# Performance work log

Measured on AMD Instinct MI355X. Metric: run time of the kernel, lower is better.

The kernel has to match this reference:

```python
import jax, jax.numpy as jnp
import numpy as np
from jax import lax

DIM = 512
BATCH = 8
SEQ = 2048
LR = 0.1      # learning_rate (eta)
DECAY = 0.9   # decay_rate (lambda)


def setup_inputs() -> dict:
    key = jax.random.key(0)
    ks = jax.random.split(key, 5)
    scale = DIM ** -0.5
    return {
        "x": jax.random.normal(ks[0], (BATCH, SEQ, DIM), dtype=jnp.float32),
        "Wk": jax.random.normal(ks[1], (DIM, DIM), dtype=jnp.float32) * scale,
        "bk": jnp.zeros((DIM,), dtype=jnp.float32),
        "Wv": jax.random.normal(ks[2], (DIM, DIM), dtype=jnp.float32) * scale,
        "bv": jnp.zeros((DIM,), dtype=jnp.float32),
        "Wq": jax.random.normal(ks[3], (DIM, DIM), dtype=jnp.float32) * scale,
        "bq": jnp.zeros((DIM,), dtype=jnp.float32),
        "Wo": jax.random.normal(ks[4], (DIM, DIM), dtype=jnp.float32) * scale,
        "bo": jnp.zeros((DIM,), dtype=jnp.float32),
    }


def reference(x, Wk, bk, Wv, bv, Wq, bq, Wo, bo):
    B, S, D = x.shape
    # dense projections over all tokens at once
    k = x @ Wk + bk  # (B,S,D)
    v = x @ Wv + bv
    q = x @ Wq + bq

    state0 = jnp.zeros((B, D, D), dtype=x.dtype)

    def step(state, kvq):
        k_t, v_t, q_t = kvq                                  # each (B,D)
        mem = jnp.einsum('bd,bde->be', q_t, state)           # read BEFORE update
        new_state = DECAY * state + LR * jnp.einsum('bd,be->bde', k_t, v_t)
        return new_state, mem

    # scan over time: move seq axis to front
    kT = jnp.swapaxes(k, 0, 1)  # (S,B,D)
    vT = jnp.swapaxes(v, 0, 1)
    qT = jnp.swapaxes(q, 0, 1)
    final_state, mems = lax.scan(step, state0, (kT, vT, qT))  # mems (S,B,D)

    outputs = jnp.swapaxes(mems, 0, 1)                        # (B,S,D)
    out = outputs @ Wo + bo
    return out, final_state
```

## Files before the change

### kernel.cpp

```cpp
#include <hip/hip_runtime.h>
#include <math.h>


#define DIMD 512
#define SEQL 2048
#define LRC 0.1f
#define LAM64 1.1790184577738602e-3f
#define LAM128 1.3900845237714473e-6f
#define L2LAM -0.15200309344504997f

#define KVQ_ELEMS ((size_t)16384 * 512)
#define WSLAB ((size_t)512 * 512)

typedef __attribute__((ext_vector_type(8))) short bf16x8;
typedef __attribute__((ext_vector_type(4))) float f32x4;

__device__ __forceinline__ unsigned short f2bf(float f) {
  unsigned int u = __float_as_uint(f);
  u += 0x7FFFu + ((u >> 16) & 1u);
  return (unsigned short)(u >> 16);
}

__device__ __forceinline__ void gload16(const unsigned short* g, char* l) {
  __builtin_amdgcn_global_load_lds(
      (const __attribute__((address_space(1))) unsigned int*)g,
      (__attribute__((address_space(3))) unsigned int*)l, 16, 0, 0);
}

__global__ __launch_bounds__(256) void prep(
    const float* __restrict__ x, unsigned short* __restrict__ Abf,
    const float* __restrict__ Wq, const float* __restrict__ Wk,
    const float* __restrict__ Wv, const float* __restrict__ Wo,
    unsigned short* __restrict__ T) {
  const int blk = blockIdx.x;
  if (blk < 8192) {
    const size_t idx = ((size_t)blk * 256 + threadIdx.x) * 4;
    float4 v = *(const float4*)(x + idx);
    ushort4 u;
    u.x = f2bf(v.x); u.y = f2bf(v.y); u.z = f2bf(v.z); u.w = f2bf(v.w);
    *(ushort4*)(Abf + idx) = u;
    return;
  }
  const int r2 = blk - 8192;
  const int z = r2 >> 8;
  const int rem = r2 & 255;
  const int nb = (rem & 15) * 32, kb = (rem >> 4) * 32;
  const float* W = (z == 0) ? Wq : (z == 1) ? Wk : (z == 2) ? Wv : Wo;
  unsigned short* Tz = T + (size_t)z * WSLAB;
  __shared__ float tl[32][33];
  const int r = threadIdx.x >> 5, c = threadIdx.x & 31;
#pragma unroll
  for (int i = 0; i < 4; ++i)
    tl[r + i * 8][c] = W[(size_t)(kb + r + i * 8) * 512 + nb + c];
  __syncthreads();
#pragma unroll
  for (int i = 0; i < 4; ++i)
    Tz[(size_t)(nb + r + i * 8) * 512 + kb + c] = f2bf(tl[c][r + i * 8]);
}

template <int EMODE>
__global__ __launch_bounds__(256) void mfma_gemm(
    const unsigned short* __restrict__ A, int astr,
    const unsigned short* __restrict__ T0, const unsigned short* __restrict__ T1,
    const unsigned short* __restrict__ T2, int tstr,
    const float* __restrict__ b0, const float* __restrict__ b1,
    const float* __restrict__ b2,
    float* __restrict__ Cf,
    unsigned short* __restrict__ qh, unsigned short* __restrict__ kh,
    unsigned short* __restrict__ khT, unsigned short* __restrict__ vTp,
    int nkt) {
  const int z = blockIdx.z;
  const unsigned short* T = (z == 0) ? T0 : (z == 1) ? T1 : T2;
  const float* bias = (z == 0) ? b0 : (z == 1) ? b1 : b2;

  const int m0 = blockIdx.x * 128;
  const int n0 = blockIdx.y * 128;
  const int tid = threadIdx.x;
  const int lane = tid & 63;
  const int w = tid >> 6;
  const int wm = (w & 1) * 64;
  const int wn = (w >> 1) * 64;

  __shared__ __align__(16) char smem[EMODE == 0 ? 35840 : 32768];

  f32x4 acc[4][4];
  const f32x4 zf = {0.f, 0.f, 0.f, 0.f};
#pragma unroll
  for (int i = 0; i < 4; ++i)
#pragma unroll
    for (int j = 0; j < 4; ++j) acc[i][j] = zf;

  const int lr = lane >> 3;
  const int lo3 = lane & 7;
  const int xr = lo3 ^ lr;
  const int mbase = w * 32 + lr * 2 + (xr >> 2);
  const int kel = (xr & 3) * 8;
  const unsigned short* Ag = A + (size_t)(m0 + mbase) * astr + kel;
  const unsigned short* Tg = T + (size_t)(n0 + mbase) * tstr + kel;

#define ISSUE(KT, BUF)                                                     \
  {                                                                        \
    char* ab = smem + (BUF) * 8192 + w * 2048;                             \
    char* bb_ = smem + 16384 + (BUF) * 8192 + w * 2048;                    \
    _Pragma("unroll") for (int c = 0; c < 2; ++c) {                        \
      gload16(Ag + (size_t)(c * 16) * astr + (KT) * 32, ab + c * 1024);    \
      gload16(Tg + (size_t)(c * 16) * tstr + (KT) * 32, bb_ + c * 1024);   \
    }                                                                      \
  }

  const int fr = lane & 15;
  const int fg = lane >> 4;
  const int foff = ((((fr & 1) << 6) | (fg << 4)) ^ (((fr >> 1) & 7) << 4));
  const int aline = (wm >> 1) + (fr >> 1);
  const int bline = (wn >> 1) + (fr >> 1);

  ISSUE(0, 0);
  int bb = 0;
  for (int kt = 0; kt < nkt; ++kt) {
    if (kt + 1 < nkt) {
      ISSUE(kt + 1, bb ^ 1);
      asm volatile("s_waitcnt vmcnt(4)" ::: "memory");
    } else {
      asm volatile("s_waitcnt vmcnt(0)" ::: "memory");
    }
    __builtin_amdgcn_sched_barrier(0);
    __builtin_amdgcn_s_barrier();
    const char* pa = smem + bb * 8192 + aline * 128 + foff;
    const char* pb = smem + 16384 + bb * 8192 + bline * 128 + foff;
    bf16x8 af[4], bfr[4];
#pragma unroll
    for (int mi = 0; mi < 4; ++mi) af[mi] = *(const bf16x8*)(pa + mi * 1024);
#pragma unroll
    for (int ni = 0; ni < 4; ++ni) bfr[ni] = *(const bf16x8*)(pb + ni * 1024);
#pragma unroll
    for (int mi = 0; mi < 4; ++mi)
#pragma unroll
      for (int ni = 0; ni < 4; ++ni)
        acc[mi][ni] = __builtin_amdgcn_mfma_f32_16x16x32_bf16(
            af[mi], bfr[ni], acc[mi][ni], 0, 0, 0);
    __builtin_amdgcn_s_barrier();
    __builtin_amdgcn_sched_barrier(0);
    bb ^= 1;
  }
#undef ISSUE

  const int orow = fg * 4;

  if (EMODE == 1) {
#pragma unroll
    for (int ni = 0; ni < 4; ++ni) {
      const int col = n0 + wn + ni * 16 + fr;
      const float bi = bias[col];
#pragma unroll
      for (int mi = 0; mi < 4; ++mi) {
        float* cp = Cf + (size_t)(m0 + wm + mi * 16 + orow) * 512 + col;
#pragma unroll
        for (int r = 0; r < 4; ++r) cp[(size_t)r * 512] = acc[mi][ni][r] + bi;
      }
    }
    return;
  }

  __syncthreads();
  unsigned short* cl = (unsigned short*)smem;
  const size_t batch = (size_t)(m0 >> 11);
  const int tl = m0 & 2047;

  if (z <= 1) {
#pragma unroll
    for (int ni = 0; ni < 4; ++ni) {
      const int col = wn + ni * 16 + fr;
      const float bi = bias[n0 + col];
#pragma unroll
      for (int mi = 0; mi < 4; ++mi) {
#pragma unroll
        for (int r = 0; r < 4; ++r) {
          const int row = wm + mi * 16 + orow + r;
          float v = acc[mi][ni][r] + bi;
          v *= (z == 0) ? exp2f(L2LAM * (float)(row & 63))
                        : LRC * exp2f(-L2LAM * (float)((row & 63) + 1));
          cl[row * 136 + col] = f2bf(v);
        }
      }
    }
    __syncthreads();
    {
      const int row = tid >> 1, half = tid & 1;
      unsigned short* dst = (z == 0 ? qh : kh) +
          (size_t)(m0 + row) * DIMD + n0 + half * 64;
      const unsigned short* sp = cl + row * 136 + half * 64;
#pragma unroll
      for (int j = 0; j < 8; ++j)
        *(float4*)(dst + j * 8) = *(const float4*)(sp + j * 8);
    }
  }
  if (z >= 1) {
    __syncthreads();
#pragma unroll
    for (int ni = 0; ni < 4; ++ni) {
      const int col = wn + ni * 16 + fr;
      const float bi = bias[n0 + col];
#pragma unroll
      for (int mi = 0; mi < 4; ++mi) {
#pragma unroll
        for (int r = 0; r < 4; ++r) {
          const int row = wm + mi * 16 + orow + r;
          float v = acc[mi][ni][r] + bi;
          if (z == 1) v *= LRC * exp2f(-L2LAM * (float)((row & 63) + 1));
          cl[col * 136 + row] = f2bf(v);
        }
      }
    }
    __syncthreads();
    {
      const int col = tid >> 1, half = tid & 1;
      unsigned short* dstT = (z == 1 ? khT : vTp) + batch * DIMD * SEQL +
          (size_t)(n0 + col) * SEQL + tl + half * 64;
      const unsigned short* sp = cl + col * 136 + half * 64;
#pragma unroll
      for (int j = 0; j < 8; ++j)
        *(float4*)(dstT + j * 8) = *(const float4*)(sp + j * 8);
    }
  }
}

__global__ __launch_bounds__(256) void battn(
    const unsigned short* __restrict__ qh, const unsigned short* __restrict__ kh,
    const unsigned short* __restrict__ vTp, const unsigned short* __restrict__ khT,
    unsigned short* __restrict__ mbf, float* __restrict__ fstate) {
  const int blk = blockIdx.x;
  const int tid = threadIdx.x;
  const int lane = tid & 63;
  const int w = tid >> 6;
  const int fr = lane & 15;
  const int fg = lane >> 4;

  __shared__ __align__(16) char Kl[65536];
  __shared__ __align__(16) unsigned short Pl[64 * 72];

  if (blk >= 512) {
    const int b2 = blk - 512;
    const int b = b2 & 7;
    const int slab = b2 >> 3;
    const int e0g = slab * 32;
    const int wd0 = w * 128;
    const unsigned short* kTb = khT + (size_t)b * DIMD * SEQL;
    const unsigned short* vTb = vTp + (size_t)b * DIMD * SEQL;

    f32x4 S[8][2];
    const f32x4 zf = {0.f, 0.f, 0.f, 0.f};
#pragma unroll
    for (int mi = 0; mi < 8; ++mi)
#pragma unroll
      for (int ni = 0; ni < 2; ++ni) S[mi][ni] = zf;

#pragma unroll
    for (int tb = 29; tb < 32; ++tb) {
      const int t0 = tb * 64;
#pragma unroll
      for (int ks2 = 0; ks2 < 2; ++ks2) {
        bf16x8 aK[8], bV[2];
#pragma unroll
        for (int mi = 0; mi < 8; ++mi)
          aK[mi] = *(const bf16x8*)(kTb + (size_t)(wd0 + mi * 16 + fr) * SEQL +
                                    t0 + ks2 * 32 + fg * 8);
#pragma unroll
        for (int ni = 0; ni < 2; ++ni)
          bV[ni] = *(const bf16x8*)(vTb + (size_t)(e0g + ni * 16 + fr) * SEQL +
                                    t0 + ks2 * 32 + fg * 8);
#pragma unroll
        for (int mi = 0; mi < 8; ++mi)
#pragma unroll
          for (int ni = 0; ni < 2; ++ni)
            S[mi][ni] = __builtin_amdgcn_mfma_f32_16x16x32_bf16(aK[mi], bV[ni],
                                                                S[mi][ni], 0, 0, 0);
      }
#pragma unroll
      for (int mi = 0; mi < 8; ++mi)
#pragma unroll
        for (int ni = 0; ni < 2; ++ni) {
          S[mi][ni][0] *= LAM64;
          S[mi][ni][1] *= LAM64;
          S[mi][ni][2] *= LAM64;
          S[mi][ni][3] *= LAM64;
        }
    }
    float* fs = fstate + (size_t)b * DIMD * DIMD;
#pragma unroll
    for (int mi = 0; mi < 8; ++mi)
#pragma unroll
      for (int ni = 0; ni < 2; ++ni) {
        const int e = e0g + ni * 16 + fr;
#pragma unroll
        for (int r = 0; r < 4; ++r) {
          const int d = w * 128 + mi * 16 + fg * 4 + r;
          fs[(size_t)d * DIMD + e] = S[mi][ni][r];
        }
      }
    return;
  }

  const int b = blk & 7;
  const int rest = blk >> 3;
  const int j = rest & 31;
  const int h = rest >> 5;
  const int t0 = j * 64;
  const int e0g = h * 256;
  const int wt0 = w * 16;
  const int nstartb = (j >= 2) ? 0 : (2 - j);

  const unsigned short* qb = qh + (size_t)b * SEQL * DIMD;
  const unsigned short* kb = kh + (size_t)b * SEQL * DIMD;
  const unsigned short* vTb = vTp + (size_t)b * DIMD * SEQL;
  unsigned short* mb = mbf + (size_t)b * SEQL * DIMD;

  const int selem = lane * 8;

#define STAGE(S0)                                                            \
  {                                                                          \
    _Pragma("unroll") for (int c = 0; c < 16; ++c) {                         \
      const int row = w * 16 + c;                                            \
      gload16(kb + (size_t)((S0) + row) * DIMD + (selem ^ ((row & 7) << 3)), \
              Kl + row * 1024);                                              \
    }                                                                        \
  }

  STAGE(t0 - 128 + nstartb * 64);

  bf16x8 aq[16];
  {
    const unsigned short* qrow = qb + (size_t)(t0 + wt0 + fr) * DIMD + fg * 8;
#pragma unroll
    for (int ks = 0; ks < 16; ++ks) aq[ks] = *(const bf16x8*)(qrow + ks * 32);
  }

  f32x4 mem[4][4];
  const f32x4 zf = {0.f, 0.f, 0.f, 0.f};
#pragma unroll
  for (int mi = 0; mi < 4; ++mi)
#pragma unroll
    for (int ni = 0; ni < 4; ++ni) mem[mi][ni] = zf;

  const int ew = e0g + w * 64;

  for (int sb = nstartb; sb < 3; ++sb) {
    const int s0 = t0 - 128 + sb * 64;
    __syncthreads();

    f32x4 P[4];
#pragma unroll
    for (int ni = 0; ni < 4; ++ni) P[ni] = zf;
#pragma unroll
    for (int ks = 0; ks < 16; ++ks) {
      bf16x8 bK[4];
#pragma unroll
      for (int ni = 0; ni < 4; ++ni) {
        const int row = ni * 16 + fr;
        bK[ni] = *(const bf16x8*)(Kl + row * 1024 +
                                  ((ks * 64 + fg * 16) ^ ((row & 7) << 4)));
      }
#pragma unroll
      for (int ni = 0; ni < 4; ++ni)
        P[ni] = __builtin_amdgcn_mfma_f32_16x16x32_bf16(aq[ks], bK[ni], P[ni], 0, 0, 0);
    }

#pragma unroll
    for (int ni = 0; ni < 4; ++ni) {
      const int s = ni * 16 + fr;
#pragma unroll
      for (int r = 0; r < 4; ++r) {
        const int t = wt0 + fg * 4 + r;
        float v = (sb == 0) ? P[ni][r] * LAM128
                : (sb == 1) ? P[ni][r] * LAM64
                            : ((s < t) ? P[ni][r] : 0.f);
        Pl[t * 72 + s] = f2bf(v);
      }
    }
    __syncthreads();
    if (sb + 1 < 3) STAGE(s0 + 64);

#pragma unroll
    for (int ks2 = 0; ks2 < 2; ++ks2) {
      bf16x8 ap[4];
#pragma unroll
      for (int mi = 0; mi < 4; ++mi)
        ap[mi] = *(const bf16x8*)(Pl + (mi * 16 + fr) * 72 + ks2 * 32 + fg * 8);
      const int tk = s0 + ks2 * 32 + fg * 8;
#pragma unroll
      for (int ni = 0; ni < 4; ++ni) {
        bf16x8 bV = *(const bf16x8*)(vTb + (size_t)(ew + ni * 16 + fr) * SEQL + tk);
#pragma unroll
        for (int mi = 0; mi < 4; ++mi)
          mem[mi][ni] = __builtin_amdgcn_mfma_f32_16x16x32_bf16(ap[mi], bV,
                                                               mem[mi][ni], 0, 0, 0);
      }
    }
  }
#undef STAGE

#pragma unroll
  for (int mi = 0; mi < 4; ++mi)
#pragma unroll
    for (int ni = 0; ni < 4; ++ni)
#pragma unroll
      for (int r = 0; r < 4; ++r) {
        const int t = t0 + mi * 16 + fg * 4 + r;
        mb[(size_t)t * DIMD + ew + ni * 16 + fr] = f2bf(mem[mi][ni][r]);
      }
}

extern "C" void kernel_launch(void* const* d_in, const int* in_sizes, int n_in,
                              void* d_out, int out_size, void* d_ws,
                              size_t ws_size, hipStream_t stream) {
  const float* x  = (const float*)d_in[0];
  const float* Wk = (const float*)d_in[1];
  const float* bk = (const float*)d_in[2];
  const float* Wv = (const float*)d_in[3];
  const float* bv = (const float*)d_in[4];
  const float* Wq = (const float*)d_in[5];
  const float* bq = (const float*)d_in[6];
  const float* Wo = (const float*)d_in[7];
  const float* bo = (const float*)d_in[8];

  float* outp = (float*)d_out;
  float* fstate = outp + KVQ_ELEMS;

  unsigned short* qhb = (unsigned short*)d_ws;
  unsigned short* khb = qhb + KVQ_ELEMS;
  unsigned short* khT = qhb + 2 * KVQ_ELEMS;
  unsigned short* vTp = qhb + 3 * KVQ_ELEMS;
  unsigned short* mbf = qhb + 4 * KVQ_ELEMS;
  unsigned short* WT  = qhb + 5 * KVQ_ELEMS;

  unsigned short* Abf = (unsigned short*)d_out;

  prep<<<dim3(9216), 256, 0, stream>>>(x, Abf, Wq, Wk, Wv, Wo, WT);
  mfma_gemm<0><<<dim3(128, 4, 3), 256, 0, stream>>>(
      Abf, 512, WT , WT + WSLAB , WT + 2 * WSLAB , 512,
      bq, bk, bv, nullptr, qhb, khb, khT, vTp, 16);
  battn<<<dim3(640), 256, 0, stream>>>(qhb, khb, vTp, khT, mbf, fstate);
  mfma_gemm<1><<<dim3(128, 4, 1), 256, 0, stream>>>(
      mbf, 512, WT + 3 * WSLAB, WT + 3 * WSLAB, WT + 3 * WSLAB, 512,
      bo, bo, bo, outp, nullptr, nullptr, nullptr, nullptr, 16);
}
```

Before: 123.4 us.

## Retile projection GEMMs to 256x256 blocks with 512 threads and swizzled grid

Replaces the 128x128, 256-thread GEMM with a 256x256 tile computed by 8 waves, using a K-step of 64, double-buffered 128KB of LDS and a 1D swizzled block order. Prefetch of the next K tile is split across the MFMA sub-steps, and s_setprio is raised around the MFMA bursts. The epilogue writes through LDS in two 128-column chunks. The transposed K copy is now written only for the last 256 tokens of each batch, which cuts store traffic. The cost is lower occupancy and a heavier LDS footprint per block.

```diff
diff --git a/kernel.cpp b/kernel.cpp
--- a/kernel.cpp
+++ b/kernel.cpp
@@ -59,100 +59,119 @@
 }
 
 template <int EMODE>
-__global__ __launch_bounds__(256) void mfma_gemm(
-    const unsigned short* __restrict__ A, int astr,
-    const unsigned short* __restrict__ T0, const unsigned short* __restrict__ T1,
-    const unsigned short* __restrict__ T2, int tstr,
+__global__ __launch_bounds__(512, 2) void mfma_gemm(
+    const unsigned short* __restrict__ A,
+    const unsigned short* __restrict__ T,
     const float* __restrict__ b0, const float* __restrict__ b1,
     const float* __restrict__ b2,
     float* __restrict__ Cf,
     unsigned short* __restrict__ qh, unsigned short* __restrict__ kh,
-    unsigned short* __restrict__ khT, unsigned short* __restrict__ vTp,
-    int nkt) {
-  const int z = blockIdx.z;
-  const unsigned short* T = (z == 0) ? T0 : (z == 1) ? T1 : T2;
+    unsigned short* __restrict__ khT, unsigned short* __restrict__ vTp) {
+  __shared__ __align__(16) char smem[131072];
+
+  const int wg = blockIdx.x;
+  int swz, mt, nt;
+  if (EMODE == 0) {
+    swz = (wg & 7) * 48 + (wg >> 3);
+    mt = swz / 6; nt = swz - mt * 6;
+  } else {
+    swz = (wg & 7) * 16 + (wg >> 3);
+    mt = swz >> 1; nt = swz & 1;
+  }
+  const int z = (EMODE == 0) ? (nt >> 1) : 0;
+  const int nloc0 = (EMODE == 0) ? ((nt & 1) * 256) : (nt * 256);
+  const int m0 = mt * 256;
+  const unsigned short* Tz = T + (size_t)z * WSLAB;
   const float* bias = (z == 0) ? b0 : (z == 1) ? b1 : b2;
 
-  const int m0 = blockIdx.x * 128;
-  const int n0 = blockIdx.y * 128;
   const int tid = threadIdx.x;
   const int lane = tid & 63;
   const int w = tid >> 6;
-  const int wm = (w & 1) * 64;
-  const int wn = (w >> 1) * 64;
-
-  __shared__ __align__(16) char smem[EMODE == 0 ? 35840 : 32768];
-
-  f32x4 acc[4][4];
+  const int fr = lane & 15, fg = lane >> 4;
+  const int wm = (w >> 2) * 128;
+  const int wn = (w & 3) * 64;
+
+  const int srow = tid >> 3;
+  const int ecolx = ((tid & 7) * 8) ^ ((srow & 7) * 8);
+  const unsigned short* As = A + (size_t)(m0 + srow) * DIMD + ecolx;
+  const unsigned short* Bs = Tz + (size_t)(nloc0 + srow) * DIMD + ecolx;
+  char* const sdA = smem + w * 1024;
+  char* const sdB = smem + 65536 + w * 1024;
+
+#define STAGE_A(KT, BUF)                                                  \
+  { char* d = sdA + (BUF) * 32768;                                        \
+    _Pragma("unroll") for (int s = 0; s < 4; ++s)                         \
+      gload16(As + (size_t)(s * 64) * DIMD + (KT) * 64, d + s * 8192); }
+#define STAGE_B(KT, BUF)                                                  \
+  { char* d = sdB + (BUF) * 32768;                                        \
+    _Pragma("unroll") for (int s = 0; s < 4; ++s)                         \
+      gload16(Bs + (size_t)(s * 64) * DIMD + (KT) * 64, d + s * 8192); }
+
+  const int xsw = (fr & 7) << 4;
+  const int offk0 = (fg * 16) ^ xsw;
+  const int offk1 = (64 + fg * 16) ^ xsw;
+  const int arow_off = (wm + fr) * 128;
+  const int brow_off = (wn + fr) * 128;
+
+  f32x4 acc[8][4];
   const f32x4 zf = {0.f, 0.f, 0.f, 0.f};
 #pragma unroll
-  for (int i = 0; i < 4; ++i)
+  for (int i = 0; i < 8; ++i)
 #pragma unroll
     for (int j = 0; j < 4; ++j) acc[i][j] = zf;
 
-  const int lr = lane >> 3;
-  const int lo3 = lane & 7;
-  const int xr = lo3 ^ lr;
-  const int mbase = w * 32 + lr * 2 + (xr >> 2);
-  const int kel = (xr & 3) * 8;
-  const unsigned short* Ag = A + (size_t)(m0 + mbase) * astr + kel;
-  const unsigned short* Tg = T + (size_t)(n0 + mbase) * tstr + kel;
-
-#define ISSUE(KT, BUF)                                                     \
-  {                                                                        \
-    char* ab = smem + (BUF) * 8192 + w * 2048;                             \
-    char* bb_ = smem + 16384 + (BUF) * 8192 + w * 2048;                    \
-    _Pragma("unroll") for (int c = 0; c < 2; ++c) {                        \
-      gload16(Ag + (size_t)(c * 16) * astr + (KT) * 32, ab + c * 1024);    \
-      gload16(Tg + (size_t)(c * 16) * tstr + (KT) * 32, bb_ + c * 1024);   \
-    }                                                                      \
-  }
-
-  const int fr = lane & 15;
-  const int fg = lane >> 4;
-  const int foff = ((((fr & 1) << 6) | (fg << 4)) ^ (((fr >> 1) & 7) << 4));
-  const int aline = (wm >> 1) + (fr >> 1);
-  const int bline = (wn >> 1) + (fr >> 1);
-
-  ISSUE(0, 0);
-  int bb = 0;
-  for (int kt = 0; kt < nkt; ++kt) {
-    if (kt + 1 < nkt) {
-      ISSUE(kt + 1, bb ^ 1);
-      asm volatile("s_waitcnt vmcnt(4)" ::: "memory");
-    } else {
-      asm volatile("s_waitcnt vmcnt(0)" ::: "memory");
-    }
-    __builtin_amdgcn_sched_barrier(0);
-    __builtin_amdgcn_s_barrier();
-    const char* pa = smem + bb * 8192 + aline * 128 + foff;
-    const char* pb = smem + 16384 + bb * 8192 + bline * 128 + foff;
-    bf16x8 af[4], bfr[4];
-#pragma unroll
-    for (int mi = 0; mi < 4; ++mi) af[mi] = *(const bf16x8*)(pa + mi * 1024);
-#pragma unroll
-    for (int ni = 0; ni < 4; ++ni) bfr[ni] = *(const bf16x8*)(pb + ni * 1024);
-#pragma unroll
-    for (int mi = 0; mi < 4; ++mi)
-#pragma unroll
-      for (int ni = 0; ni < 4; ++ni)
-        acc[mi][ni] = __builtin_amdgcn_mfma_f32_16x16x32_bf16(
-            af[mi], bfr[ni], acc[mi][ni], 0, 0, 0);
-    __builtin_amdgcn_s_barrier();
-    __builtin_amdgcn_sched_barrier(0);
-    bb ^= 1;
-  }
-#undef ISSUE
+  STAGE_A(0, 0);
+  STAGE_B(0, 0);
+  __syncthreads();
+
+  for (int kt = 0; kt < 8; ++kt) {
+    const int cur = kt & 1;
+    const char* pa = smem + cur * 32768 + arow_off;
+    const char* pb = smem + 65536 + cur * 32768 + brow_off;
+    bf16x8 bfr[4];
+#pragma unroll
+    for (int q = 0; q < 4; ++q) {
+      const int qm = q & 1;
+      const int offk = (q >> 1) ? offk1 : offk0;
+      if (qm == 0) {
+#pragma unroll
+        for (int ni = 0; ni < 4; ++ni)
+          bfr[ni] = *(const bf16x8*)(pb + ni * 2048 + offk);
+      }
+      bf16x8 af[4];
+#pragma unroll
+      for (int i = 0; i < 4; ++i)
+        af[i] = *(const bf16x8*)(pa + (qm * 4 + i) * 2048 + offk);
+      if (q == 0 && kt < 7) STAGE_A(kt + 1, cur ^ 1);
+      if (q == 1 && kt < 7) STAGE_B(kt + 1, cur ^ 1);
+      __builtin_amdgcn_s_barrier();
+      __builtin_amdgcn_s_setprio(1);
+#pragma unroll
+      for (int i = 0; i < 4; ++i)
+#pragma unroll
+        for (int ni = 0; ni < 4; ++ni)
+          acc[qm * 4 + i][ni] = __builtin_amdgcn_mfma_f32_16x16x32_bf16(
+              af[i], bfr[ni], acc[qm * 4 + i][ni], 0, 0, 0);
+      __builtin_amdgcn_s_setprio(0);
+      if (q < 3) {
+        __builtin_amdgcn_s_barrier();
+      } else {
+        __syncthreads();
+      }
+    }
+  }
+#undef STAGE_A
+#undef STAGE_B
 
   const int orow = fg * 4;
 
   if (EMODE == 1) {
 #pragma unroll
     for (int ni = 0; ni < 4; ++ni) {
-      const int col = n0 + wn + ni * 16 + fr;
-      const float bi = bias[col];
-#pragma unroll
-      for (int mi = 0; mi < 4; ++mi) {
+      const int col = nloc0 + wn + ni * 16 + fr;
+      const float bi = b0[col];
+#pragma unroll
+      for (int mi = 0; mi < 8; ++mi) {
         float* cp = Cf + (size_t)(m0 + wm + mi * 16 + orow) * 512 + col;
 #pragma unroll
         for (int r = 0; r < 4; ++r) cp[(size_t)r * 512] = acc[mi][ni][r] + bi;
@@ -161,65 +180,81 @@
     return;
   }
 
-  __syncthreads();
   unsigned short* cl = (unsigned short*)smem;
   const size_t batch = (size_t)(m0 >> 11);
   const int tl = m0 & 2047;
+  const int chw = (w >> 1) & 1;
+  const int lcb = (w & 1) * 64;
 
   if (z <= 1) {
-#pragma unroll
-    for (int ni = 0; ni < 4; ++ni) {
-      const int col = wn + ni * 16 + fr;
-      const float bi = bias[n0 + col];
-#pragma unroll
-      for (int mi = 0; mi < 4; ++mi) {
-#pragma unroll
-        for (int r = 0; r < 4; ++r) {
-          const int row = wm + mi * 16 + orow + r;
-          float v = acc[mi][ni][r] + bi;
-          v *= (z == 0) ? exp2f(L2LAM * (float)(row & 63))
-                        : LRC * exp2f(-L2LAM * (float)((row & 63) + 1));
-          cl[row * 136 + col] = f2bf(v);
+    __syncthreads();
+#pragma unroll
+    for (int ch = 0; ch < 2; ++ch) {
+      if (ch) __syncthreads();
+      if (chw == ch) {
+#pragma unroll
+        for (int ni = 0; ni < 4; ++ni) {
+          const int lcol = lcb + ni * 16 + fr;
+          const float bi = bias[nloc0 + ch * 128 + lcol];
+#pragma unroll
+          for (int mi = 0; mi < 8; ++mi) {
+#pragma unroll
+            for (int r = 0; r < 4; ++r) {
+              const int row = wm + mi * 16 + orow + r;
+              float v = acc[mi][ni][r] + bi;
+              v *= (z == 0) ? exp2f(L2LAM * (float)(row & 63))
+                            : LRC * exp2f(-L2LAM * (float)((row & 63) + 1));
+              cl[row * 136 + lcol] = f2bf(v);
+            }
+          }
         }
       }
-    }
+      __syncthreads();
+      {
+        const int row = tid >> 1, seg = tid & 1;
+        unsigned short* dst = (z == 0 ? qh : kh) + (size_t)(m0 + row) * DIMD +
+            nloc0 + ch * 128 + seg * 64;
+        const unsigned short* sp = cl + row * 136 + seg * 64;
+#pragma unroll
+        for (int j2 = 0; j2 < 8; ++j2)
+          *(float4*)(dst + j2 * 8) = *(const float4*)(sp + j2 * 8);
+      }
+    }
+  }
+
+  if (z == 2 || (z == 1 && tl == 1792)) {
     __syncthreads();
-    {
-      const int row = tid >> 1, half = tid & 1;
-      unsigned short* dst = (z == 0 ? qh : kh) +
-          (size_t)(m0 + row) * DIMD + n0 + half * 64;
-      const unsigned short* sp = cl + row * 136 + half * 64;
-#pragma unroll
-      for (int j = 0; j < 8; ++j)
-        *(float4*)(dst + j * 8) = *(const float4*)(sp + j * 8);
-    }
-  }
-  if (z >= 1) {
-    __syncthreads();
-#pragma unroll
-    for (int ni = 0; ni < 4; ++ni) {
-      const int col = wn + ni * 16 + fr;
-      const float bi = bias[n0 + col];
-#pragma unroll
-      for (int mi = 0; mi < 4; ++mi) {
-#pragma unroll
-        for (int r = 0; r < 4; ++r) {
-          const int row = wm + mi * 16 + orow + r;
-          float v = acc[mi][ni][r] + bi;
-          if (z == 1) v *= LRC * exp2f(-L2LAM * (float)((row & 63) + 1));
-          cl[col * 136 + row] = f2bf(v);
+#pragma unroll
+    for (int ch = 0; ch < 2; ++ch) {
+      if (ch) __syncthreads();
+      if (chw == ch) {
+#pragma unroll
+        for (int ni = 0; ni < 4; ++ni) {
+          const int lcol = lcb + ni * 16 + fr;
+          const float bi = bias[nloc0 + ch * 128 + lcol];
+#pragma unroll
+          for (int mi = 0; mi < 8; ++mi) {
+#pragma unroll
+            for (int r = 0; r < 4; ++r) {
+              const int row = wm + mi * 16 + orow + r;
+              float v = acc[mi][ni][r] + bi;
+              if (z == 1) v *= LRC * exp2f(-L2LAM * (float)((row & 63) + 1));
+              cl[lcol * 264 + row] = f2bf(v);
+            }
+          }
         }
       }
-    }
-    __syncthreads();
-    {
-      const int col = tid >> 1, half = tid & 1;
-      unsigned short* dstT = (z == 1 ? khT : vTp) + batch * DIMD * SEQL +
-          (size_t)(n0 + col) * SEQL + tl + half * 64;
-      const unsigned short* sp = cl + col * 136 + half * 64;
-#pragma unroll
-      for (int j = 0; j < 8; ++j)
-        *(float4*)(dstT + j * 8) = *(const float4*)(sp + j * 8);
+      __syncthreads();
+      {
+        const int col = tid >> 2, rseg = tid & 3;
+        unsigned short* dstT = (z == 1 ? khT : vTp) +
+            batch * ((size_t)DIMD * SEQL) +
+            (size_t)(nloc0 + ch * 128 + col) * SEQL + tl + rseg * 64;
+        const unsigned short* sp = cl + col * 264 + rseg * 64;
+#pragma unroll
+        for (int j2 = 0; j2 < 8; ++j2)
+          *(float4*)(dstT + j2 * 8) = *(const float4*)(sp + j2 * 8);
+      }
     }
   }
 }
@@ -435,11 +470,9 @@
   unsigned short* Abf = (unsigned short*)d_out;
 
   prep<<<dim3(9216), 256, 0, stream>>>(x, Abf, Wq, Wk, Wv, Wo, WT);
-  mfma_gemm<0><<<dim3(128, 4, 3), 256, 0, stream>>>(
-      Abf, 512, WT , WT + WSLAB , WT + 2 * WSLAB , 512,
-      bq, bk, bv, nullptr, qhb, khb, khT, vTp, 16);
+  mfma_gemm<0><<<dim3(384), 512, 0, stream>>>(
+      Abf, WT, bq, bk, bv, nullptr, qhb, khb, khT, vTp);
   battn<<<dim3(640), 256, 0, stream>>>(qhb, khb, vTp, khT, mbf, fstate);
-  mfma_gemm<1><<<dim3(128, 4, 1), 256, 0, stream>>>(
-      mbf, 512, WT + 3 * WSLAB, WT + 3 * WSLAB, WT + 3 * WSLAB, 512,
-      bo, bo, bo, outp, nullptr, nullptr, nullptr, nullptr, 16);
-}
+  mfma_gemm<1><<<dim3(128), 512, 0, stream>>>(
+      mbf, WT + 3 * WSLAB, bo, bo, bo, outp, nullptr, nullptr, nullptr, nullptr);
+}
```

After: 168.1 us. 36.2% more time.
